# Kernel tuning notes

Hardware: AMD Instinct MI355X
Metric: run time of the kernel (lower is better)

## Reference

```python
import jax, jax.numpy as jnp
import numpy as np

HEADS, HEAD_SIZE, FREQS, MAX_PERIOD = 16, 64, 256, 10000
D_MODEL = 1024
NEG_INF = -1e9


def sinusoid_embedding(seq_len, frequencies, max_period):
    # Interleaved sin/cos sinusoid table, shape (seq_len, frequencies).
    pos = np.arange(seq_len, dtype=np.float64)[:, None]
    idx = np.arange(frequencies)[None, :]
    inv_freq = max_period ** (-(idx // 2 * 2) / frequencies)
    angle = pos * inv_freq
    table = np.where(idx % 2 == 0, np.sin(angle), np.cos(angle))
    return table.astype(np.float32)


def relative_causal(scores):
    # scores: (b, n, q, v) with v indexing relative distance d = q - k.
    # Returns a[..., q, k] = scores[..., q, q - k] (k > q entries are masked later).
    L = scores.shape[-1]
    d = jnp.clip(jnp.arange(L)[:, None] - jnp.arange(L)[None, :], 0, L - 1)  # (q, k)
    return jnp.take_along_axis(scores, d[None, None, :, :], axis=-1)


def setup_inputs() -> dict:
    key = jax.random.key(0)
    ks = jax.random.split(key, 4)
    u = np.sqrt(3.0)
    inp = jax.random.normal(ks[0], (2, 2048, D_MODEL), dtype=jnp.float32)
    qkv = jax.random.uniform(ks[1], (D_MODEL, 3, HEADS, HEAD_SIZE), jnp.float32, -u, u)
    q_bias = jnp.zeros((HEADS, HEAD_SIZE), jnp.float32)
    positional = jax.random.uniform(ks[2], (FREQS, HEADS, HEAD_SIZE), jnp.float32, -u, u)
    out_kernel = jax.random.uniform(ks[3], (HEADS * HEAD_SIZE, D_MODEL), jnp.float32, -u, u)
    out_bias = jnp.zeros((D_MODEL,), jnp.float32)
    return {"input": inp, "qkv": qkv, "q_bias": q_bias, "positional": positional,
            "out_kernel": out_kernel, "out_bias": out_bias}


def reference(input, qkv, q_bias, positional, out_kernel, out_bias):
    b, s, x = input.shape
    n, h = HEADS, HEAD_SIZE
    # QKV projection with unit-scaling forward factor.
    w = qkv * (3.0 * x * h * n) ** -0.25
    q, k, v = jnp.einsum('bsx,xAnh->Abnsh', input, w)  # each (b, n, s, h)
    q = q + q_bias[:, None, :]
    # Content scores.
    a = jnp.einsum('bnqh,bnkh->bnqk', q, k) * h ** -0.5
    # Relative-positional scores (Transformer-XL style).
    sins = jnp.asarray(np.sqrt(2.0) * sinusoid_embedding(s, FREQS, MAX_PERIOD))
    emb = jnp.einsum('sf,fnh->nsh', sins, positional * FREQS ** -0.5)
    pos_scores = jnp.einsum('bnqh,nvh->bnqv', q, emb) * h ** -0.5
    a = a + relative_causal(pos_scores)
    # Causal mask + softmax.
    mask = jnp.tril(jnp.ones((s, s), dtype=bool))
    a = jax.nn.softmax(jnp.where(mask, a, NEG_INF), axis=-1)
    # Weighted sum and output projection (Dense, scale_for='both').
    o = jnp.einsum('bnqk,bnkh->bqnh', a, v).reshape(b, s, n * h)
    fan_in, fan_out = out_kernel.shape
    out = o @ (out_kernel * (fan_in * fan_out) ** -0.25) + out_bias
    return out
```

## Files before the change

### kernel.cpp

```cpp
#include <hip/hip_runtime.h>
#include <math.h>

#define BATCH 2
#define SEQ 2048
#define DMODEL 1024
#define HEADS 16
#define HSIZE 64
#define FREQS 256
#define NH 1024
#define QKVN 3072

typedef __bf16 bf16;
typedef __bf16 bf16x8 __attribute__((ext_vector_type(8)));
typedef float f32x4 __attribute__((ext_vector_type(4)));

static __device__ __forceinline__ unsigned short bf16_bits(float v) {
    bf16 b = (bf16)v; return __builtin_bit_cast(unsigned short, b);
}

static __device__ __forceinline__ void gload16(const void* g, void* l) {
    __builtin_amdgcn_global_load_lds(
        (const __attribute__((address_space(1))) unsigned int*)g,
        (__attribute__((address_space(3))) unsigned int*)l, 16, 0, 0);
}

__global__ void sins_kernel(bf16* __restrict__ sins) {
    int i = blockIdx.x * blockDim.x + threadIdx.x;
    int s = i >> 8;
    int f = i & 255;
    double e = -(double)((f >> 1) << 1) / (double)FREQS;
    double invf = pow(10000.0, e);
    double ang = (double)s * invf;
    double v = (f & 1) ? cos(ang) : sin(ang);
    sins[i] = (bf16)(float)(1.4142135623730951 * v);
}

__global__ void cast_bf16(const float* __restrict__ src, bf16* __restrict__ dst, int n4) {
    int i = blockIdx.x * blockDim.x + threadIdx.x;
    if (i >= n4) return;
    float4 v = ((const float4*)src)[i];
    ushort4 o;
    o.x = bf16_bits(v.x); o.y = bf16_bits(v.y);
    o.z = bf16_bits(v.z); o.w = bf16_bits(v.w);
    ((ushort4*)dst)[i] = o;
}

__global__ __launch_bounds__(256) void transpose_cast(
    const float* __restrict__ src, bf16* __restrict__ dst, int R, int C)
{
    __shared__ float tile[32][33];
    const int tx = threadIdx.x & 31, ty = threadIdx.x >> 5;
    const int c0 = blockIdx.x * 32, r0 = blockIdx.y * 32;
#pragma unroll
    for (int i = 0; i < 4; i++)
        tile[ty + i * 8][tx] = src[(size_t)(r0 + ty + i * 8) * C + c0 + tx];
    __syncthreads();
#pragma unroll
    for (int i = 0; i < 4; i++)
        dst[(size_t)(c0 + ty + i * 8) * R + r0 + tx] = (bf16)tile[tx][ty + i * 8];
}

template<int EPI>
__global__ __launch_bounds__(256) void mfma_gemm(
    const bf16* __restrict__ A, const bf16* __restrict__ Bt,
    int K, float alpha, const float* __restrict__ bias,
    float* __restrict__ outf, bf16* __restrict__ ob0, bf16* __restrict__ ob1,
    bf16* __restrict__ ob2)
{
    __shared__ __align__(16) bf16 Atile[128 * 32];
    __shared__ __align__(16) bf16 Btile[128 * 32];

    const int t    = threadIdx.x;
    const int lane = t & 63;
    const int w    = t >> 6;
    const int quad = lane >> 4;
    const int l16  = lane & 15;
    const int m0   = blockIdx.y * 128;
    const int n0   = blockIdx.x * 128;
    const int wm   = (w >> 1) * 64;
    const int wn   = (w & 1) * 64;
    const bool swapv = (EPI == 1) && (n0 >= 2048);

    const int rS  = t >> 2;
    const int cS  = (t & 3) ^ ((rS >> 1) & 3);
    const bf16* ag0 = A  + (size_t)(m0 + rS) * K + cS * 8;
    const bf16* ag1 = A  + (size_t)(m0 + rS + 64) * K + cS * 8;
    const bf16* bg0 = Bt + (size_t)(n0 + rS) * K + cS * 8;
    const bf16* bg1 = Bt + (size_t)(n0 + rS + 64) * K + cS * 8;
    bf16* al0 = Atile + t * 8;
    bf16* al1 = Atile + (t + 256) * 8;
    bf16* bl0 = Btile + t * 8;
    bf16* bl1 = Btile + (t + 256) * 8;

    int aoff[4], boff[4];
#pragma unroll
    for (int mi = 0; mi < 4; ++mi) {
        int r = wm + mi * 16 + l16;
        aoff[mi] = r * 32 + ((quad ^ ((r >> 1) & 3)) * 8);
    }
#pragma unroll
    for (int ni = 0; ni < 4; ++ni) {
        int r = wn + ni * 16 + l16;
        boff[ni] = r * 32 + ((quad ^ ((r >> 1) & 3)) * 8);
    }

    f32x4 acc[4][4] = {};

    for (int kk = 0; kk < K; kk += 32) {
        __syncthreads();
        gload16(ag0, al0); gload16(ag1, al1);
        gload16(bg0, bl0); gload16(bg1, bl1);
        ag0 += 32; ag1 += 32; bg0 += 32; bg1 += 32;
        __syncthreads();

        bf16x8 af[4], bfr[4];
#pragma unroll
        for (int mi = 0; mi < 4; ++mi) af[mi] = *(const bf16x8*)(Atile + aoff[mi]);
#pragma unroll
        for (int ni = 0; ni < 4; ++ni) bfr[ni] = *(const bf16x8*)(Btile + boff[ni]);

        if (!swapv) {
#pragma unroll
            for (int mi = 0; mi < 4; ++mi)
#pragma unroll
                for (int ni = 0; ni < 4; ++ni)
                    acc[mi][ni] = __builtin_amdgcn_mfma_f32_16x16x32_bf16(
                        af[mi], bfr[ni], acc[mi][ni], 0, 0, 0);
        } else {
#pragma unroll
            for (int mi = 0; mi < 4; ++mi)
#pragma unroll
                for (int ni = 0; ni < 4; ++ni)
                    acc[mi][ni] = __builtin_amdgcn_mfma_f32_16x16x32_bf16(
                        bfr[ni], af[mi], acc[mi][ni], 0, 0, 0);
        }
    }

    if constexpr (EPI == 0) {
#pragma unroll
        for (int mi = 0; mi < 4; ++mi)
#pragma unroll
            for (int ni = 0; ni < 4; ++ni) {
                int col = n0 + wn + ni * 16 + l16;
                float bb = bias[col];
#pragma unroll
                for (int rg = 0; rg < 4; ++rg) {
                    int row = m0 + wm + mi * 16 + quad * 4 + rg;
                    outf[(size_t)row * NH + col] = acc[mi][ni][rg] * alpha + bb;
                }
            }
    } else if constexpr (EPI == 1) {
        if (n0 >= 2048) {
#pragma unroll
            for (int mi = 0; mi < 4; ++mi)
#pragma unroll
                for (int ni = 0; ni < 4; ++ni) {
                    int mcol = m0 + wm + mi * 16 + l16;
                    int bb = mcol >> 11, s = mcol & 2047;
#pragma unroll
                    for (int rg = 0; rg < 4; ++rg) {
                        int hg = n0 + wn + ni * 16 + quad * 4 + rg;
                        int head = (hg & 1023) >> 6, h = hg & 63;
                        int ss = s ^ ((h & 7) << 3);
                        ob2[((size_t)((bb * 16 + head) * 64 + h)) * SEQ + ss] =
                            (bf16)(acc[mi][ni][rg] * alpha);
                    }
                }
        } else {
            const int whichk = (n0 >= 1024);
#pragma unroll
            for (int mi = 0; mi < 4; ++mi)
#pragma unroll
                for (int ni = 0; ni < 4; ++ni) {
                    int cg   = (n0 + wn + ni * 16 + l16) & 1023;
                    int head = cg >> 6, h = cg & 63;
                    float qbv = whichk ? 0.0f : bias[cg];
#pragma unroll
                    for (int rg = 0; rg < 4; ++rg) {
                        int row = m0 + wm + mi * 16 + quad * 4 + rg;
                        int bb = row >> 11, s = row & 2047;
                        float v = acc[mi][ni][rg] * alpha;
                        if (whichk) {
                            int hs = h ^ ((s & 7) << 3);
                            ob1[((size_t)((bb * 16 + head) * SEQ + s)) * 64 + hs] = (bf16)v;
                        } else {
                            ob0[((size_t)((bb * 16 + head) * SEQ + s)) * 64 + h] =
                                (bf16)((v + qbv) * 0.125f);
                        }
                    }
                }
        }
    } else {
#pragma unroll
        for (int mi = 0; mi < 4; ++mi)
#pragma unroll
            for (int ni = 0; ni < 4; ++ni) {
                int col = n0 + wn + ni * 16 + l16;
                int head = col >> 6, h = col & 63;
#pragma unroll
                for (int rg = 0; rg < 4; ++rg) {
                    int d = m0 + wm + mi * 16 + quad * 4 + rg;
                    int hs = h ^ (((d + 63) & 7) << 3);
                    ob0[((size_t)(head * SEQ + d)) * 64 + hs] =
                        (bf16)(acc[mi][ni][rg] * alpha);
                }
            }
    }
}

__global__ __launch_bounds__(256, 2) void attn_kernel(
    const bf16* __restrict__ Qb, const bf16* __restrict__ Kb,
    const bf16* __restrict__ Vtb, const bf16* __restrict__ Eb,
    bf16* __restrict__ o)
{
    __shared__ __align__(16) bf16 Ks[2][4096];
    __shared__ __align__(16) bf16 Vts[2][4096];
    __shared__ __align__(16) bf16 Es[256 * 64];
    __shared__ __align__(16) bf16 PS[4][16][72];

    const int t    = threadIdx.x;
    const int lane = t & 63;
    const int w    = t >> 6;
    const int quad = lane >> 4;
    const int l16  = lane & 15;

    const int bx = blockIdx.x;
    const int b  = bx >> 4, n = bx & 15;
    const int yy = blockIdx.y;
    const int qc = (yy < 8) ? (15 - 2 * yy) : (2 * yy - 16);
    const int q0 = qc * 128;
    const int KT = 2 * qc + 2;
    const int qw0 = q0 + 16 * w;
    const int qw1 = qw0 + 64;

    const bf16* __restrict__ Qp = Qb  + (size_t)bx * SEQ * 64;
    const bf16* __restrict__ Kp = Kb  + (size_t)bx * SEQ * 64;
    const bf16* __restrict__ Vp = Vtb + (size_t)bx * SEQ * 64;
    const bf16* __restrict__ Ep = Eb  + (size_t)n  * SEQ * 64;

    const int key8 = (l16 & 7) << 3;
    const int ec0  = ((quad * 8) ^ key8) * 2;
    const int ec1  = ((32 + quad * 8) ^ key8) * 2;

    bf16x8 qf[2][2];
    qf[0][0] = *(const bf16x8*)(Qp + (size_t)(qw0 + l16) * 64 + quad * 8);
    qf[0][1] = *(const bf16x8*)(Qp + (size_t)(qw0 + l16) * 64 + 32 + quad * 8);
    qf[1][0] = *(const bf16x8*)(Qp + (size_t)(qw1 + l16) * 64 + quad * 8);
    qf[1][1] = *(const bf16x8*)(Qp + (size_t)(qw1 + l16) * 64 + 32 + quad * 8);

    int dsta[4];
    bool condp[4];
#pragma unroll
    for (int rg = 0; rg < 4; ++rg) {
        int rr   = quad * 4 + rg;
        int l16c = (rr + 15 - l16) & 15;
        dsta[rg]  = ((lane & 48) + l16c) << 2;
        condp[rg] = rr > l16c;
    }

    f32x4 O[2][4] = {};
    float lsum[2][4] = {};

    {
        gload16(Kp + t * 8,        (char*)Ks[0] + t * 16);
        gload16(Kp + 2048 + t * 8, (char*)Ks[0] + 4096 + t * 16);
        gload16(Vp + (size_t)(t >> 3) * SEQ + (t & 7) * 8,        (char*)Vts[0] + t * 16);
        gload16(Vp + (size_t)((t >> 3) + 32) * SEQ + (t & 7) * 8, (char*)Vts[0] + 4096 + t * 16);
        const long D0 = (long)q0 - 63;
#pragma unroll
        for (int g = 0; g < 6; ++g)
            gload16(Ep + (D0 + 32 * g) * 64 + t * 8, (char*)Es + g * 4096 + t * 16);
    }

    for (int kt = 0; kt < KT; ++kt) {
        const int k0 = kt * 64;
        __syncthreads();

        const int nt = kt + 1;
        if (nt < KT) {
            bf16* kd = Ks[nt & 1];
            bf16* vd = Vts[nt & 1];
            const bf16* ksrc = Kp + nt * 4096;
            gload16(ksrc + t * 8,        (char*)kd + t * 16);
            gload16(ksrc + 2048 + t * 8, (char*)kd + 4096 + t * 16);
            gload16(Vp + (size_t)(t >> 3) * SEQ + nt * 64 + (t & 7) * 8,
                    (char*)vd + t * 16);
            gload16(Vp + (size_t)((t >> 3) + 32) * SEQ + nt * 64 + (t & 7) * 8,
                    (char*)vd + 4096 + t * 16);
            const long d0 = (long)q0 - nt * 64 - 63;
            const int rI = (-64 * nt) & 255;
            gload16(Ep + d0 * 64 + t * 8,        (char*)Es + rI * 128 + t * 16);
            gload16(Ep + (d0 + 32) * 64 + t * 8, (char*)Es + rI * 128 + 4096 + t * 16);
        }

        const char* kb = (const char*)Ks[kt & 1];
        const char* vb = (const char*)Vts[kt & 1];
        bf16x8 kf[4][2], vf[4][2];
#pragma unroll
        for (int j = 0; j < 4; ++j) {
            const char* kp = kb + (j * 16 + l16) * 128;
            kf[j][0] = *(const bf16x8*)(kp + ec0);
            kf[j][1] = *(const bf16x8*)(kp + ec1);
            const char* vp = vb + (j * 16 + l16) * 128;
            vf[j][0] = *(const bf16x8*)(vp + ec0);
            vf[j][1] = *(const bf16x8*)(vp + ec1);
        }

        const bool last = (nt == KT);
#pragma unroll
        for (int c = 0; c < 2; ++c) {
            if (c == 0 && last) continue;
            const int qwc = c ? qw1 : qw0;

            f32x4 pa[5];
            const int rb = 16 * w + 64 * c - k0;
#pragma unroll
            for (int jj = 0; jj < 5; ++jj) {
                const char* ep = (const char*)Es + ((rb + 16 * jj + l16) & 255) * 128;
                bf16x8 e0 = *(const bf16x8*)(ep + ec0);
                bf16x8 e1 = *(const bf16x8*)(ep + ec1);
                f32x4 a = {0, 0, 0, 0};
                a = __builtin_amdgcn_mfma_f32_16x16x32_bf16(qf[c][1], e1, a, 0, 0, 0);
                a = __builtin_amdgcn_mfma_f32_16x16x32_bf16(qf[c][0], e0, a, 0, 0, 0);
                pa[jj] = a;
            }

            f32x4 S[4];
#pragma unroll
            for (int j = 0; j < 4; ++j) {
                f32x4 a = {0, 0, 0, 0};
                a = __builtin_amdgcn_mfma_f32_16x16x32_bf16(qf[c][1], kf[j][1], a, 0, 0, 0);
                a = __builtin_amdgcn_mfma_f32_16x16x32_bf16(qf[c][0], kf[j][0], a, 0, 0, 0);
                S[j] = a;
            }

#pragma unroll
            for (int j = 0; j < 4; ++j) {
#pragma unroll
                for (int rg = 0; rg < 4; ++rg) {
                    float vsel = condp[rg] ? pa[4 - j][rg] : pa[3 - j][rg];
                    int pv = __builtin_amdgcn_ds_permute(dsta[rg], __float_as_int(vsel));
                    float sv = S[j][rg] + __int_as_float(pv);
                    bool valid = (k0 + j * 16 + l16) <= (qwc + quad * 4 + rg);
                    S[j][rg] = valid ? __expf(sv) : 0.0f;
                }
            }
#pragma unroll
            for (int rg = 0; rg < 4; ++rg)
                lsum[c][rg] += S[0][rg] + S[1][rg] + S[2][rg] + S[3][rg];

#pragma unroll
            for (int j = 0; j < 4; ++j)
#pragma unroll
                for (int rg = 0; rg < 4; ++rg)
                    PS[w][quad * 4 + rg][j * 16 + l16] = (bf16)S[j][rg];
            bf16x8 pf0 = *(const bf16x8*)(&PS[w][l16][quad * 8]);
            bf16x8 pf1 = *(const bf16x8*)(&PS[w][l16][32 + quad * 8]);

#pragma unroll
            for (int j4 = 0; j4 < 4; ++j4) {
                O[c][j4] = __builtin_amdgcn_mfma_f32_16x16x32_bf16(pf1, vf[j4][1], O[c][j4], 0, 0, 0);
                O[c][j4] = __builtin_amdgcn_mfma_f32_16x16x32_bf16(pf0, vf[j4][0], O[c][j4], 0, 0, 0);
            }
        }
    }

#pragma unroll
    for (int c = 0; c < 2; ++c) {
#pragma unroll
        for (int rg = 0; rg < 4; ++rg) {
            float s = lsum[c][rg];
            s += __shfl_xor(s, 1);
            s += __shfl_xor(s, 2);
            s += __shfl_xor(s, 4);
            s += __shfl_xor(s, 8);
            float inv = 1.0f / s;
            int q = (c ? qw1 : qw0) + quad * 4 + rg;
            size_t ro = ((size_t)(b * SEQ + q)) * NH + n * 64;
            o[ro +  0 + l16] = (bf16)(O[c][0][rg] * inv);
            o[ro + 16 + l16] = (bf16)(O[c][1][rg] * inv);
            o[ro + 32 + l16] = (bf16)(O[c][2][rg] * inv);
            o[ro + 48 + l16] = (bf16)(O[c][3][rg] * inv);
        }
    }
}

extern "C" void kernel_launch(void* const* d_in, const int* in_sizes, int n_in,
                              void* d_out, int out_size, void* d_ws, size_t ws_size,
                              hipStream_t stream) {
    const float* inp        = (const float*)d_in[0];
    const float* qkv_w      = (const float*)d_in[1];
    const float* q_bias     = (const float*)d_in[2];
    const float* positional = (const float*)d_in[3];
    const float* out_kernel = (const float*)d_in[4];
    const float* out_bias   = (const float*)d_in[5];

    char* p = (char*)d_ws;
    auto alloc = [&](size_t bytes) {
        char* q = p; p += (bytes + 255) & ~(size_t)255; return q;
    };
    bf16* qbuf    = (bf16*)alloc((size_t)BATCH * HEADS * SEQ * HSIZE * 2);
    bf16* kbuf    = (bf16*)alloc((size_t)BATCH * HEADS * SEQ * HSIZE * 2);
    bf16* vtbuf   = (bf16*)alloc((size_t)BATCH * HEADS * SEQ * HSIZE * 2);
    bf16* embT    = (bf16*)alloc((size_t)HEADS * SEQ * HSIZE * 2);
    bf16* sins_bf = (bf16*)alloc((size_t)SEQ * FREQS * 2);
    bf16* obuf    = (bf16*)alloc((size_t)BATCH * SEQ * NH * 2);
    bf16* a_bf    = (bf16*)alloc((size_t)BATCH * SEQ * DMODEL * 2);
    bf16* wt_qkv  = (bf16*)alloc((size_t)QKVN * DMODEL * 2);
    bf16* wt_out  = (bf16*)alloc((size_t)NH * DMODEL * 2);
    bf16* wt_pos  = (bf16*)alloc((size_t)NH * FREQS * 2);

    const float qkv_scale = (float)pow(3.0 * DMODEL * HSIZE * HEADS, -0.25);
    const float emb_scale = 0.0625f;
    const float out_scale = 0.03125f;

    cast_bf16<<<(BATCH * SEQ * DMODEL / 4 + 255) / 256, 256, 0, stream>>>(
        inp, a_bf, BATCH * SEQ * DMODEL / 4);
    transpose_cast<<<dim3(QKVN / 32, DMODEL / 32), 256, 0, stream>>>(
        qkv_w, wt_qkv, DMODEL, QKVN);
    transpose_cast<<<dim3(NH / 32, DMODEL / 32), 256, 0, stream>>>(
        out_kernel, wt_out, DMODEL, NH);
    transpose_cast<<<dim3(NH / 32, FREQS / 32), 256, 0, stream>>>(
        positional, wt_pos, FREQS, NH);
    sins_kernel<<<SEQ * FREQS / 256, 256, 0, stream>>>(sins_bf);

    mfma_gemm<1><<<dim3(24, 32), 256, 0, stream>>>(
        a_bf, wt_qkv, DMODEL, qkv_scale, q_bias, nullptr, qbuf, kbuf, vtbuf);
    mfma_gemm<3><<<dim3(8, 16), 256, 0, stream>>>(
        sins_bf, wt_pos, FREQS, emb_scale, nullptr, nullptr, embT, nullptr, nullptr);

    attn_kernel<<<dim3(32, 16), 256, 0, stream>>>(
        qbuf, kbuf, vtbuf, embT, obuf);

    mfma_gemm<0><<<dim3(8, 32), 256, 0, stream>>>(
        obuf, wt_out, DMODEL, out_scale, out_bias, (float*)d_out,
        nullptr, nullptr, nullptr);
}
```

Baseline: 278.1 us.

## Merge prep kernels, fuse embedding GEMM into QKV GEMM, double-buffer GEMM tiles

Five prep launches (input cast, three weight transposes, sinusoid table) become one prep_kernel whose work is split by block-index ranges. The positional-embedding GEMM is folded into the QKV GEMM grid as extra columns of blocks, and the now-unused EPI 3 path is removed. The GEMM mainloop gains double-buffered LDS tiles so the next K-slice loads while the current one computes, removing one barrier per iteration. This cuts launch overhead and improves load/compute overlap, at the cost of more LDS and some idle blocks in the merged grid.

Measured after the change: 263.6 us. -5.2%, faster.

```diff
diff --git a/kernel.cpp b/kernel.cpp
--- a/kernel.cpp
+++ b/kernel.cpp
@@ -24,33 +24,50 @@
         (__attribute__((address_space(3))) unsigned int*)l, 16, 0, 0);
 }
 
-__global__ void sins_kernel(bf16* __restrict__ sins) {
-    int i = blockIdx.x * blockDim.x + threadIdx.x;
-    int s = i >> 8;
-    int f = i & 255;
-    double e = -(double)((f >> 1) << 1) / (double)FREQS;
-    double invf = pow(10000.0, e);
-    double ang = (double)s * invf;
-    double v = (f & 1) ? cos(ang) : sin(ang);
-    sins[i] = (bf16)(float)(1.4142135623730951 * v);
-}
-
-__global__ void cast_bf16(const float* __restrict__ src, bf16* __restrict__ dst, int n4) {
-    int i = blockIdx.x * blockDim.x + threadIdx.x;
-    if (i >= n4) return;
-    float4 v = ((const float4*)src)[i];
-    ushort4 o;
-    o.x = bf16_bits(v.x); o.y = bf16_bits(v.y);
-    o.z = bf16_bits(v.z); o.w = bf16_bits(v.w);
-    ((ushort4*)dst)[i] = o;
-}
-
-__global__ __launch_bounds__(256) void transpose_cast(
-    const float* __restrict__ src, bf16* __restrict__ dst, int R, int C)
+__global__ __launch_bounds__(256) void prep_kernel(
+    const float* __restrict__ inp, const float* __restrict__ qkv_w,
+    const float* __restrict__ out_kernel, const float* __restrict__ positional,
+    bf16* __restrict__ a_bf, bf16* __restrict__ wt_qkv,
+    bf16* __restrict__ wt_out, bf16* __restrict__ wt_pos,
+    bf16* __restrict__ sins_bf)
 {
     __shared__ float tile[32][33];
-    const int tx = threadIdx.x & 31, ty = threadIdx.x >> 5;
-    const int c0 = blockIdx.x * 32, r0 = blockIdx.y * 32;
+    const int id = blockIdx.x, t = threadIdx.x;
+
+    if (id < 4096) {
+        int i = id * 256 + t;
+        float4 v = ((const float4*)inp)[i];
+        ushort4 o;
+        o.x = bf16_bits(v.x); o.y = bf16_bits(v.y);
+        o.z = bf16_bits(v.z); o.w = bf16_bits(v.w);
+        ((ushort4*)a_bf)[i] = o;
+        return;
+    }
+    if (id < 6144) {
+        int i = (id - 4096) * 256 + t;
+        int s = i >> 8, f = i & 255;
+        double e = -(double)((f >> 1) << 1) / (double)FREQS;
+        double invf = pow(10000.0, e);
+        double ang = (double)s * invf;
+        double v = (f & 1) ? cos(ang) : sin(ang);
+        sins_bf[i] = (bf16)(float)(1.4142135623730951 * v);
+        return;
+    }
+    int id2 = id - 6144;
+    const float* src; bf16* dst; int R, C, c0, r0;
+    if (id2 < 3072) {
+        src = qkv_w; dst = wt_qkv; R = 1024; C = 3072;
+        c0 = (id2 % 96) * 32; r0 = (id2 / 96) * 32;
+    } else if (id2 < 4096) {
+        id2 -= 3072;
+        src = out_kernel; dst = wt_out; R = 1024; C = 1024;
+        c0 = (id2 & 31) * 32; r0 = (id2 >> 5) * 32;
+    } else {
+        id2 -= 4096;
+        src = positional; dst = wt_pos; R = 256; C = 1024;
+        c0 = (id2 & 31) * 32; r0 = (id2 >> 5) * 32;
+    }
+    const int tx = t & 31, ty = t >> 5;
 #pragma unroll
     for (int i = 0; i < 4; i++)
         tile[ty + i * 8][tx] = src[(size_t)(r0 + ty + i * 8) * C + c0 + tx];
@@ -65,32 +82,40 @@
     const bf16* __restrict__ A, const bf16* __restrict__ Bt,
     int K, float alpha, const float* __restrict__ bias,
     float* __restrict__ outf, bf16* __restrict__ ob0, bf16* __restrict__ ob1,
-    bf16* __restrict__ ob2)
+    bf16* __restrict__ ob2,
+    const bf16* __restrict__ A2, const bf16* __restrict__ Bt2,
+    bf16* __restrict__ ob3, float alpha2)
 {
-    __shared__ __align__(16) bf16 Atile[128 * 32];
-    __shared__ __align__(16) bf16 Btile[128 * 32];
+    __shared__ __align__(16) bf16 Atile[2][128 * 32];
+    __shared__ __align__(16) bf16 Btile[2][128 * 32];
 
     const int t    = threadIdx.x;
     const int lane = t & 63;
     const int w    = t >> 6;
     const int quad = lane >> 4;
     const int l16  = lane & 15;
-    const int m0   = blockIdx.y * 128;
-    const int n0   = blockIdx.x * 128;
     const int wm   = (w >> 1) * 64;
     const int wn   = (w & 1) * 64;
-    const bool swapv = (EPI == 1) && (n0 >= 2048);
-
-    const int rS  = t >> 2;
-    const int cS  = (t & 3) ^ ((rS >> 1) & 3);
-    const bf16* ag0 = A  + (size_t)(m0 + rS) * K + cS * 8;
-    const bf16* ag1 = A  + (size_t)(m0 + rS + 64) * K + cS * 8;
-    const bf16* bg0 = Bt + (size_t)(n0 + rS) * K + cS * 8;
-    const bf16* bg1 = Bt + (size_t)(n0 + rS + 64) * K + cS * 8;
-    bf16* al0 = Atile + t * 8;
-    bf16* al1 = Atile + (t + 256) * 8;
-    bf16* bl0 = Btile + t * 8;
-    bf16* bl1 = Btile + (t + 256) * 8;
+
+    bool embp = false;
+    int m0 = blockIdx.y * 128, n0 = blockIdx.x * 128, Kl = K;
+    const bf16* Ap = A; const bf16* Btp = Bt; float al = alpha;
+    if constexpr (EPI == 1) {
+        if (blockIdx.x >= 24) {
+            if (blockIdx.y >= 16) return;
+            embp = true;
+            n0 = (blockIdx.x - 24) * 128;
+            Kl = FREQS; Ap = A2; Btp = Bt2; al = alpha2;
+        }
+    }
+    const bool swapv = (EPI == 1) && !embp && (n0 >= 2048);
+
+    const int rS = t >> 2;
+    const int cS = (t & 3) ^ ((rS >> 1) & 3);
+    const bf16* ag0 = Ap  + (size_t)(m0 + rS) * Kl + cS * 8;
+    const bf16* ag1 = ag0 + (size_t)64 * Kl;
+    const bf16* bg0 = Btp + (size_t)(n0 + rS) * Kl + cS * 8;
+    const bf16* bg1 = bg0 + (size_t)64 * Kl;
 
     int aoff[4], boff[4];
 #pragma unroll
@@ -104,20 +129,30 @@
         boff[ni] = r * 32 + ((quad ^ ((r >> 1) & 3)) * 8);
     }
 
+    gload16(ag0, (char*)Atile[0] + t * 16);
+    gload16(ag1, (char*)Atile[0] + 4096 + t * 16);
+    gload16(bg0, (char*)Btile[0] + t * 16);
+    gload16(bg1, (char*)Btile[0] + 4096 + t * 16);
+
+    const int nK = Kl >> 5;
     f32x4 acc[4][4] = {};
 
-    for (int kk = 0; kk < K; kk += 32) {
+    for (int kk = 0; kk < nK; ++kk) {
         __syncthreads();
-        gload16(ag0, al0); gload16(ag1, al1);
-        gload16(bg0, bl0); gload16(bg1, bl1);
-        ag0 += 32; ag1 += 32; bg0 += 32; bg1 += 32;
-        __syncthreads();
-
+        if (kk + 1 < nK) {
+            ag0 += 32; ag1 += 32; bg0 += 32; bg1 += 32;
+            char* ad = (char*)Atile[(kk + 1) & 1];
+            char* bd = (char*)Btile[(kk + 1) & 1];
+            gload16(ag0, ad + t * 16); gload16(ag1, ad + 4096 + t * 16);
+            gload16(bg0, bd + t * 16); gload16(bg1, bd + 4096 + t * 16);
+        }
+        const bf16* ab = Atile[kk & 1];
+        const bf16* bb = Btile[kk & 1];
         bf16x8 af[4], bfr[4];
 #pragma unroll
-        for (int mi = 0; mi < 4; ++mi) af[mi] = *(const bf16x8*)(Atile + aoff[mi]);
-#pragma unroll
-        for (int ni = 0; ni < 4; ++ni) bfr[ni] = *(const bf16x8*)(Btile + boff[ni]);
+        for (int mi = 0; mi < 4; ++mi) af[mi] = *(const bf16x8*)(ab + aoff[mi]);
+#pragma unroll
+        for (int ni = 0; ni < 4; ++ni) bfr[ni] = *(const bf16x8*)(bb + boff[ni]);
 
         if (!swapv) {
 #pragma unroll
@@ -146,11 +181,26 @@
 #pragma unroll
                 for (int rg = 0; rg < 4; ++rg) {
                     int row = m0 + wm + mi * 16 + quad * 4 + rg;
-                    outf[(size_t)row * NH + col] = acc[mi][ni][rg] * alpha + bb;
+                    outf[(size_t)row * NH + col] = acc[mi][ni][rg] * al + bb;
                 }
             }
-    } else if constexpr (EPI == 1) {
-        if (n0 >= 2048) {
+    } else {
+        if (embp) {
+#pragma unroll
+            for (int mi = 0; mi < 4; ++mi)
+#pragma unroll
+                for (int ni = 0; ni < 4; ++ni) {
+                    int col = n0 + wn + ni * 16 + l16;
+                    int head = col >> 6, h = col & 63;
+#pragma unroll
+                    for (int rg = 0; rg < 4; ++rg) {
+                        int d = m0 + wm + mi * 16 + quad * 4 + rg;
+                        int hs = h ^ (((d + 63) & 7) << 3);
+                        ob3[((size_t)(head * SEQ + d)) * 64 + hs] =
+                            (bf16)(acc[mi][ni][rg] * al);
+                    }
+                }
+        } else if (n0 >= 2048) {
 #pragma unroll
             for (int mi = 0; mi < 4; ++mi)
 #pragma unroll
@@ -163,7 +213,7 @@
                         int head = (hg & 1023) >> 6, h = hg & 63;
                         int ss = s ^ ((h & 7) << 3);
                         ob2[((size_t)((bb * 16 + head) * 64 + h)) * SEQ + ss] =
-                            (bf16)(acc[mi][ni][rg] * alpha);
+                            (bf16)(acc[mi][ni][rg] * al);
                     }
                 }
         } else {
@@ -179,7 +229,7 @@
                     for (int rg = 0; rg < 4; ++rg) {
                         int row = m0 + wm + mi * 16 + quad * 4 + rg;
                         int bb = row >> 11, s = row & 2047;
-                        float v = acc[mi][ni][rg] * alpha;
+                        float v = acc[mi][ni][rg] * al;
                         if (whichk) {
                             int hs = h ^ ((s & 7) << 3);
                             ob1[((size_t)((bb * 16 + head) * SEQ + s)) * 64 + hs] = (bf16)v;
@@ -190,21 +240,6 @@
                     }
                 }
         }
-    } else {
-#pragma unroll
-        for (int mi = 0; mi < 4; ++mi)
-#pragma unroll
-            for (int ni = 0; ni < 4; ++ni) {
-                int col = n0 + wn + ni * 16 + l16;
-                int head = col >> 6, h = col & 63;
-#pragma unroll
-                for (int rg = 0; rg < 4; ++rg) {
-                    int d = m0 + wm + mi * 16 + quad * 4 + rg;
-                    int hs = h ^ (((d + 63) & 7) << 3);
-                    ob0[((size_t)(head * SEQ + d)) * 64 + hs] =
-                        (bf16)(acc[mi][ni][rg] * alpha);
-                }
-            }
     }
 }
 
@@ -414,25 +449,17 @@
     const float emb_scale = 0.0625f;
     const float out_scale = 0.03125f;
 
-    cast_bf16<<<(BATCH * SEQ * DMODEL / 4 + 255) / 256, 256, 0, stream>>>(
-        inp, a_bf, BATCH * SEQ * DMODEL / 4);
-    transpose_cast<<<dim3(QKVN / 32, DMODEL / 32), 256, 0, stream>>>(
-        qkv_w, wt_qkv, DMODEL, QKVN);
-    transpose_cast<<<dim3(NH / 32, DMODEL / 32), 256, 0, stream>>>(
-        out_kernel, wt_out, DMODEL, NH);
-    transpose_cast<<<dim3(NH / 32, FREQS / 32), 256, 0, stream>>>(
-        positional, wt_pos, FREQS, NH);
-    sins_kernel<<<SEQ * FREQS / 256, 256, 0, stream>>>(sins_bf);
-
-    mfma_gemm<1><<<dim3(24, 32), 256, 0, stream>>>(
-        a_bf, wt_qkv, DMODEL, qkv_scale, q_bias, nullptr, qbuf, kbuf, vtbuf);
-    mfma_gemm<3><<<dim3(8, 16), 256, 0, stream>>>(
-        sins_bf, wt_pos, FREQS, emb_scale, nullptr, nullptr, embT, nullptr, nullptr);
+    prep_kernel<<<10496, 256, 0, stream>>>(
+        inp, qkv_w, out_kernel, positional, a_bf, wt_qkv, wt_out, wt_pos, sins_bf);
+
+    mfma_gemm<1><<<dim3(32, 32), 256, 0, stream>>>(
+        a_bf, wt_qkv, DMODEL, qkv_scale, q_bias, nullptr, qbuf, kbuf, vtbuf,
+        sins_bf, wt_pos, embT, emb_scale);
 
     attn_kernel<<<dim3(32, 16), 256, 0, stream>>>(
         qbuf, kbuf, vtbuf, embT, obuf);
 
     mfma_gemm<0><<<dim3(8, 32), 256, 0, stream>>>(
         obuf, wt_out, DMODEL, out_scale, out_bias, (float*)d_out,
-        nullptr, nullptr, nullptr);
-}
+        nullptr, nullptr, nullptr, nullptr, nullptr, nullptr, 0.0f);
+}
```
